# Kernel tuning notes

Hardware: AMD Instinct MI355X
Metric: run time of the kernel (lower is better)

Reference implementation:

```python
import jax, jax.numpy as jnp
import numpy as np

N = 50000      # nodes
E = 800000     # edges (before self-loops)
H = 4          # attention heads
C = 64         # hidden_dim per head
F_IN = 8       # node_features
NEG_SLOPE = 0.2  # PyG GATConv default


def setup_inputs() -> dict:
    key = jax.random.key(0)
    ks = jax.random.split(key, 16)
    def g(k, shape, fan_in):
        return (jax.random.normal(k, shape, jnp.float32) / np.sqrt(fan_in)).astype(jnp.float32)
    x = jax.random.normal(ks[0], (N, F_IN), jnp.float32)
    edge_index = jax.random.randint(ks[1], (2, E), 0, N, dtype=jnp.int32)
    # GATConv params: layer 0 maps F_IN->H*C, layers 1,2 map H*C->H*C
    W0 = g(ks[2], (F_IN, H * C), F_IN)
    Ws = g(ks[3], (2, H * C, H * C), H * C)
    att_src = g(ks[4], (3, H, C), C)
    att_dst = g(ks[5], (3, H, C), C)
    bconv = jnp.zeros((3, H * C), jnp.float32)
    # order / time predictor MLPs: Linear(256,64) -> ReLU -> Linear(64,1)
    ow1 = g(ks[6], (H * C, C), H * C); ob1 = jnp.zeros((C,), jnp.float32)
    ow2 = g(ks[7], (C, 1), C);         ob2 = jnp.zeros((1,), jnp.float32)
    tw1 = g(ks[8], (H * C, C), H * C); tb1 = jnp.zeros((C,), jnp.float32)
    tw2 = g(ks[9], (C, 1), C);         tb2 = jnp.zeros((1,), jnp.float32)
    return {"x": x, "edge_index": edge_index, "W0": W0, "Ws": Ws,
            "att_src": att_src, "att_dst": att_dst, "bconv": bconv,
            "ow1": ow1, "ob1": ob1, "ow2": ow2, "ob2": ob2,
            "tw1": tw1, "tb1": tb1, "tw2": tw2, "tb2": tb2}


def _gat_layer(h_in, src, dst, W, a_src, a_dst, b):
    """PyG-style GATConv (concat heads, eval mode, self-loops already in src/dst)."""
    h = (h_in @ W).reshape(N, H, C)                       # [N,H,C]
    al_s = jnp.einsum('nhc,hc->nh', h, a_src)             # [N,H]
    al_d = jnp.einsum('nhc,hc->nh', h, a_dst)             # [N,H]
    e = jax.nn.leaky_relu(al_s[src] + al_d[dst], NEG_SLOPE)  # [Etot,H]
    m = jax.ops.segment_max(e, dst, num_segments=N)       # segment-softmax over in-edges
    ee = jnp.exp(e - m[dst])
    den = jax.ops.segment_sum(ee, dst, num_segments=N)
    alpha = ee / den[dst]                                 # [Etot,H]
    out = jax.ops.segment_sum(h[src] * alpha[:, :, None], dst, num_segments=N)
    return out.reshape(N, H * C) + b


def reference(x, edge_index, W0, Ws, att_src, att_dst, bconv,
              ow1, ob1, ow2, ob2, tw1, tb1, tw2, tb2):
    loops = jnp.arange(N, dtype=edge_index.dtype)
    src = jnp.concatenate([edge_index[0], loops])
    dst = jnp.concatenate([edge_index[1], loops])
    h = _gat_layer(x, src, dst, W0, att_src[0], att_dst[0], bconv[0])
    h = jax.nn.relu(h)   # dropout is identity in eval
    h = _gat_layer(h, src, dst, Ws[0], att_src[1], att_dst[1], bconv[1])
    h = jax.nn.relu(h)
    h = _gat_layer(h, src, dst, Ws[1], att_src[2], att_dst[2], bconv[2])
    order_scores = jax.nn.relu(h @ ow1 + ob1) @ ow2 + ob2  # [N,1]
    time_scores = jax.nn.relu(h @ tw1 + tb1) @ tw2 + tb2   # [N,1]
    return (order_scores, time_scores)
```

## Files before the change

kernel.cpp:

```cpp
#include <hip/hip_runtime.h>
#include <hip/hip_bf16.h>
#include <hip/hip_fp16.h>

#define NN 50000
#define EE 800000
#define ET 850000
#define HH 4
#define CC 64
#define HC 256

using f16v8 = __attribute__((ext_vector_type(8))) _Float16;
using f32v4 = __attribute__((ext_vector_type(4))) float;

__device__ __forceinline__ int dst_of(const int* ei, int e) {
    return (e < EE) ? ei[EE + e] : (e - EE);
}

__device__ __forceinline__ float4 cvt_h4(uint2 raw) {
    __half2 a = *reinterpret_cast<__half2*>(&raw.x);
    __half2 b = *reinterpret_cast<__half2*>(&raw.y);
    float2 fa = __half22float2(a), fb = __half22float2(b);
    return make_float4(fa.x, fa.y, fb.x, fb.y);
}

__global__ void k_hist(const int* ei, int* cnt) {
    int e = blockIdx.x * blockDim.x + threadIdx.x;
    if (e < ET) atomicAdd(&cnt[dst_of(ei, e)], 1);
}

__global__ void k_scan1(const int* cnt, int* incl, int* bsum) {
    __shared__ int s[256];
    int i = blockIdx.x * 256 + threadIdx.x;
    int v = (i < NN) ? cnt[i] : 0;
    s[threadIdx.x] = v;
    __syncthreads();
    for (int off = 1; off < 256; off <<= 1) {
        int u = (threadIdx.x >= off) ? s[threadIdx.x - off] : 0;
        __syncthreads();
        s[threadIdx.x] += u;
        __syncthreads();
    }
    if (i < NN) incl[i] = s[threadIdx.x];
    if (threadIdx.x == 255) bsum[blockIdx.x] = s[255];
}

__global__ void k_scan2(int* bsum, int nb) {
    __shared__ int s[256];
    int v = (threadIdx.x < nb) ? bsum[threadIdx.x] : 0;
    s[threadIdx.x] = v;
    __syncthreads();
    for (int off = 1; off < 256; off <<= 1) {
        int u = (threadIdx.x >= off) ? s[threadIdx.x - off] : 0;
        __syncthreads();
        s[threadIdx.x] += u;
        __syncthreads();
    }
    if (threadIdx.x < nb) bsum[threadIdx.x] = s[threadIdx.x] - v;
}

__global__ void k_scan3(const int* cnt, const int* incl, const int* bsum,
                        int* row_ptr, int* cur) {
    int i = blockIdx.x * 256 + threadIdx.x;
    if (i < NN) {
        int excl = incl[i] - cnt[i] + bsum[blockIdx.x];
        row_ptr[i] = excl;
        cur[i] = excl;
    }
    if (blockIdx.x == 0 && threadIdx.x == 0) row_ptr[NN] = ET;
}

__global__ void k_scatter(const int* ei, int* cur, int* eidx) {
    int e = blockIdx.x * blockDim.x + threadIdx.x;
    if (e < ET) {
        int d = dst_of(ei, e);
        int pos = atomicAdd(&cur[d], 1);
        eidx[pos] = e;
    }
}

__global__ void k_prep(const float* __restrict__ Ws,
                       const float* __restrict__ ow1, const float* __restrict__ tw1,
                       __half* __restrict__ Wt, __half* __restrict__ Wh) {
    int i = blockIdx.x * 256 + threadIdx.x;
    if (i < 2 * HC * HC) {
        int m = i >> 16;
        int n = (i >> 8) & 255;
        int k = i & 255;
        Wt[i] = __float2half(Ws[m * HC * HC + k * HC + n]);
    }
    int j = i - 2 * HC * HC;
    if (j >= 0 && j < 128 * HC) {
        int c = j >> 8;
        int k = j & 255;
        float v = (c < 64) ? ow1[k * CC + c] : tw1[k * CC + (c - 64)];
        Wh[j] = __float2half(v);
    }
}

#define G0_NODES 16
__global__ __launch_bounds__(256) void k_gemm0(const float* __restrict__ x,
                                               const float* __restrict__ W0,
                                               const float* __restrict__ asrc,
                                               const float* __restrict__ adst,
                                               __half* __restrict__ hg,
                                               float* __restrict__ al_s,
                                               float* __restrict__ al_d) {
    __shared__ float sx[G0_NODES * 8];
    int t = threadIdx.x;
    int n0 = blockIdx.x * G0_NODES;
    float w[8];
#pragma unroll
    for (int k = 0; k < 8; k++) w[k] = W0[k * HC + t];
    float as = asrc[t], ad = adst[t];
    int lane = t & 63, wv = t >> 6;
    if (t < G0_NODES * 8) sx[t] = x[(size_t)n0 * 8 + t];
    __syncthreads();
    for (int ni = 0; ni < G0_NODES; ni++) {
        int n = n0 + ni;
        float acc = 0.f;
#pragma unroll
        for (int k = 0; k < 8; k++) acc += sx[ni * 8 + k] * w[k];
        hg[(size_t)n * HC + t] = __float2half(acc);
        float s = acc * as, d = acc * ad;
        for (int off = 32; off > 0; off >>= 1) {
            s += __shfl_down(s, off, 64);
            d += __shfl_down(d, off, 64);
        }
        if (lane == 0) { al_s[n * HH + wv] = s; al_d[n * HH + wv] = d; }
    }
}

#define GM 128
#define GN 128
#define GK 64
__global__ __launch_bounds__(256) void k_gemmh(const __half* __restrict__ A,
                                               const __half* __restrict__ Bt,
                                               const float* __restrict__ asrc,
                                               const float* __restrict__ adst,
                                               __half* __restrict__ hg,
                                               float* __restrict__ al_s,
                                               float* __restrict__ al_d) {
    __shared__ __half As[GM][GK + 8];
    __shared__ __half Bs[GN][GK + 8];
    int t = threadIdx.x;
    int l = t & 63, wv = t >> 6;
    int wm = wv >> 1, wn = wv & 1;
    int row0 = blockIdx.x * GM;
    int col0 = blockIdx.y * GN;
    f32v4 acc[4][4] = {};
    const __half* Ab = A + (size_t)row0 * HC;
    const __half* Bb = Bt + (size_t)col0 * HC;
    int sr = t >> 3, sc = (t & 7) * 8;
    for (int k0 = 0; k0 < HC; k0 += GK) {
#pragma unroll
        for (int i = 0; i < 4; i++) {
            int rr = sr + i * 32;
            uint4 v = {0u, 0u, 0u, 0u};
            if (row0 + rr < NN) v = *(const uint4*)(Ab + (size_t)rr * HC + k0 + sc);
            *(uint4*)&As[rr][sc] = v;
            *(uint4*)&Bs[rr][sc] = *(const uint4*)(Bb + (size_t)rr * HC + k0 + sc);
        }
        __syncthreads();
#pragma unroll
        for (int kk = 0; kk < GK; kk += 32) {
            f16v8 af[4], bf[4];
#pragma unroll
            for (int i = 0; i < 4; i++)
                af[i] = *(const f16v8*)&As[wm * 64 + i * 16 + (l & 15)][kk + (l >> 4) * 8];
#pragma unroll
            for (int j = 0; j < 4; j++)
                bf[j] = *(const f16v8*)&Bs[wn * 64 + j * 16 + (l & 15)][kk + (l >> 4) * 8];
#pragma unroll
            for (int i = 0; i < 4; i++)
#pragma unroll
                for (int j = 0; j < 4; j++)
                    acc[i][j] = __builtin_amdgcn_mfma_f32_16x16x32_f16(af[i], bf[j], acc[i][j], 0, 0, 0);
        }
        __syncthreads();
    }
    int head = (col0 >> 6) + wn;
    float va[4], vd[4];
#pragma unroll
    for (int j = 0; j < 4; j++) {
        int c = j * 16 + (l & 15);
        va[j] = asrc[head * CC + c];
        vd[j] = adst[head * CC + c];
    }
    int cbase = col0 + wn * 64 + (l & 15);
#pragma unroll
    for (int i = 0; i < 4; i++) {
#pragma unroll
        for (int v = 0; v < 4; v++) {
            int r = row0 + wm * 64 + i * 16 + (l >> 4) * 4 + v;
            bool ok = (r < NN);
            float s = 0.f, d = 0.f;
#pragma unroll
            for (int j = 0; j < 4; j++) {
                float xv = acc[i][j][v];
                s += xv * va[j];
                d += xv * vd[j];
                if (ok) hg[(size_t)r * HC + cbase + j * 16] = __float2half(xv);
            }
            s += __shfl_xor(s, 8, 16); d += __shfl_xor(d, 8, 16);
            s += __shfl_xor(s, 4, 16); d += __shfl_xor(d, 4, 16);
            s += __shfl_xor(s, 2, 16); d += __shfl_xor(d, 2, 16);
            s += __shfl_xor(s, 1, 16); d += __shfl_xor(d, 1, 16);
            if (ok && (l & 15) == 0) {
                al_s[r * HH + head] = s;
                al_d[r * HH + head] = d;
            }
        }
    }
}

__global__ __launch_bounds__(256) void k_fagg(const int* __restrict__ ei,
                                              const int* __restrict__ row_ptr,
                                              const int* __restrict__ eidx,
                                              const float* __restrict__ al_s,
                                              const float* __restrict__ al_d,
                                              const __half* __restrict__ hg,
                                              const float* __restrict__ bias,
                                              __half* __restrict__ out, int do_relu) {
    __shared__ float s_lg[4][HH][72];
    __shared__ int   s_src[4][64];
    int t = threadIdx.x;
    int wv = t >> 6, l = t & 63;
    int n = blockIdx.x * 4 + wv;
    int myh = l >> 4;
    int beg = row_ptr[n], end = row_ptr[n + 1];
    float4 ad = *(const float4*)&al_d[(size_t)n * HH];
    float m = -1e30f, den = 0.f;
    float4 acc = {0.f, 0.f, 0.f, 0.f};
    const __half* hgl = hg + l * 4;

    for (int off = beg; off < end; off += 64) {
        int csize = min(64, end - off);
        float4 lg = {-1e30f, -1e30f, -1e30f, -1e30f};
        int s = 0;
        if (l < csize) {
            int e = eidx[off + l];
            s = (e < EE) ? ei[e] : (e - EE);
            float4 as = *(const float4*)&al_s[(size_t)s * HH];
            float v;
            v = as.x + ad.x; lg.x = (v > 0.f) ? v : 0.2f * v;
            v = as.y + ad.y; lg.y = (v > 0.f) ? v : 0.2f * v;
            v = as.z + ad.z; lg.z = (v > 0.f) ? v : 0.2f * v;
            v = as.w + ad.w; lg.w = (v > 0.f) ? v : 0.2f * v;
        }
        s_src[wv][l] = s;
        s_lg[wv][0][l] = lg.x;
        s_lg[wv][1][l] = lg.y;
        s_lg[wv][2][l] = lg.z;
        s_lg[wv][3][l] = lg.w;
        float4 mx = lg;
#pragma unroll
        for (int dd = 1; dd < 64; dd <<= 1) {
            mx.x = fmaxf(mx.x, __shfl_xor(mx.x, dd, 64));
            mx.y = fmaxf(mx.y, __shfl_xor(mx.y, dd, 64));
            mx.z = fmaxf(mx.z, __shfl_xor(mx.z, dd, 64));
            mx.w = fmaxf(mx.w, __shfl_xor(mx.w, dd, 64));
        }
        float cm = (myh == 0) ? mx.x : (myh == 1) ? mx.y : (myh == 2) ? mx.z : mx.w;
        if (cm > m) {
            float sc = __expf(m - cm);
            acc.x *= sc; acc.y *= sc; acc.z *= sc; acc.w *= sc;
            den *= sc; m = cm;
        }
        const float* lgrow = s_lg[wv][myh];
        const int*   srow  = s_src[wv];
        int k = 0;
        for (; k + 8 <= csize; k += 8) {
            int si[8];
#pragma unroll
            for (int u = 0; u < 8; u++) si[u] = srow[k + u];
            uint2 rw[8];
#pragma unroll
            for (int u = 0; u < 8; u++) rw[u] = *(const uint2*)&hgl[(size_t)si[u] * HC];
            float p[8];
#pragma unroll
            for (int u = 0; u < 8; u++) p[u] = __expf(lgrow[k + u] - m);
#pragma unroll
            for (int u = 0; u < 8; u++) {
                float4 v = cvt_h4(rw[u]);
                den += p[u];
                acc.x += p[u] * v.x;
                acc.y += p[u] * v.y;
                acc.z += p[u] * v.z;
                acc.w += p[u] * v.w;
            }
        }
        for (; k + 4 <= csize; k += 4) {
            int si[4];
#pragma unroll
            for (int u = 0; u < 4; u++) si[u] = srow[k + u];
            uint2 rw[4];
#pragma unroll
            for (int u = 0; u < 4; u++) rw[u] = *(const uint2*)&hgl[(size_t)si[u] * HC];
            float p[4];
#pragma unroll
            for (int u = 0; u < 4; u++) p[u] = __expf(lgrow[k + u] - m);
#pragma unroll
            for (int u = 0; u < 4; u++) {
                float4 v = cvt_h4(rw[u]);
                den += p[u];
                acc.x += p[u] * v.x;
                acc.y += p[u] * v.y;
                acc.z += p[u] * v.z;
                acc.w += p[u] * v.w;
            }
        }
        for (; k < csize; k++) {
            float p = __expf(lgrow[k] - m);
            float4 v = cvt_h4(*(const uint2*)&hgl[(size_t)srow[k] * HC]);
            den += p;
            acc.x += p * v.x; acc.y += p * v.y; acc.z += p * v.z; acc.w += p * v.w;
        }
    }

    float4 b = *(const float4*)&bias[l * 4];
    float inv = 1.f / den;
    float4 o;
    o.x = acc.x * inv + b.x; o.y = acc.y * inv + b.y;
    o.z = acc.z * inv + b.z; o.w = acc.w * inv + b.w;
    if (do_relu) {
        o.x = fmaxf(o.x, 0.f); o.y = fmaxf(o.y, 0.f);
        o.z = fmaxf(o.z, 0.f); o.w = fmaxf(o.w, 0.f);
    }
    union { __half h[4]; uint2 u; } pk;
    pk.h[0] = __float2half(o.x); pk.h[1] = __float2half(o.y);
    pk.h[2] = __float2half(o.z); pk.h[3] = __float2half(o.w);
    *(uint2*)&out[(size_t)n * HC + l * 4] = pk.u;
}

__global__ __launch_bounds__(256) void k_headh(const __half* __restrict__ A,
                                               const __half* __restrict__ Wh,
                                               const float* __restrict__ ob1,
                                               const float* __restrict__ ow2,
                                               const float* __restrict__ ob2,
                                               const float* __restrict__ tb1,
                                               const float* __restrict__ tw2,
                                               const float* __restrict__ tb2,
                                               float* __restrict__ out) {
    __shared__ __half As[GM][GK + 8];
    __shared__ __half Bs[GN][GK + 8];
    int t = threadIdx.x;
    int l = t & 63, wv = t >> 6;
    int wm = wv >> 1, wn = wv & 1;
    int row0 = blockIdx.x * GM;
    f32v4 acc[4][4] = {};
    const __half* Ab = A + (size_t)row0 * HC;
    int sr = t >> 3, sc = (t & 7) * 8;
    for (int k0 = 0; k0 < HC; k0 += GK) {
#pragma unroll
        for (int i = 0; i < 4; i++) {
            int rr = sr + i * 32;
            uint4 v = {0u, 0u, 0u, 0u};
            if (row0 + rr < NN) v = *(const uint4*)(Ab + (size_t)rr * HC + k0 + sc);
            *(uint4*)&As[rr][sc] = v;
            *(uint4*)&Bs[rr][sc] = *(const uint4*)(Wh + (size_t)rr * HC + k0 + sc);
        }
        __syncthreads();
#pragma unroll
        for (int kk = 0; kk < GK; kk += 32) {
            f16v8 af[4], bf[4];
#pragma unroll
            for (int i = 0; i < 4; i++)
                af[i] = *(const f16v8*)&As[wm * 64 + i * 16 + (l & 15)][kk + (l >> 4) * 8];
#pragma unroll
            for (int j = 0; j < 4; j++)
                bf[j] = *(const f16v8*)&Bs[wn * 64 + j * 16 + (l & 15)][kk + (l >> 4) * 8];
#pragma unroll
            for (int i = 0; i < 4; i++)
#pragma unroll
                for (int j = 0; j < 4; j++)
                    acc[i][j] = __builtin_amdgcn_mfma_f32_16x16x32_f16(af[i], bf[j], acc[i][j], 0, 0, 0);
        }
        __syncthreads();
    }
    float b1[4], w2[4];
#pragma unroll
    for (int j = 0; j < 4; j++) {
        int c = j * 16 + (l & 15);
        b1[j] = wn ? tb1[c] : ob1[c];
        w2[j] = wn ? tw2[c] : ow2[c];
    }
    float b2 = wn ? tb2[0] : ob2[0];
#pragma unroll
    for (int i = 0; i < 4; i++) {
#pragma unroll
        for (int v = 0; v < 4; v++) {
            int r = row0 + wm * 64 + i * 16 + (l >> 4) * 4 + v;
            float s = 0.f;
#pragma unroll
            for (int j = 0; j < 4; j++)
                s += fmaxf(acc[i][j][v] + b1[j], 0.f) * w2[j];
            s += __shfl_xor(s, 8, 16);
            s += __shfl_xor(s, 4, 16);
            s += __shfl_xor(s, 2, 16);
            s += __shfl_xor(s, 1, 16);
            if ((l & 15) == 0 && r < NN)
                out[(size_t)(wn ? NN : 0) + r] = s + b2;
        }
    }
}

extern "C" void kernel_launch(void* const* d_in, const int* in_sizes, int n_in,
                              void* d_out, int out_size, void* d_ws, size_t ws_size,
                              hipStream_t stream) {
    const float* x      = (const float*)d_in[0];
    const int*   ei     = (const int*)d_in[1];
    const float* W0     = (const float*)d_in[2];
    const float* Ws     = (const float*)d_in[3];
    const float* attsrc = (const float*)d_in[4];
    const float* attdst = (const float*)d_in[5];
    const float* bconv  = (const float*)d_in[6];
    const float* ow1 = (const float*)d_in[7];
    const float* ob1 = (const float*)d_in[8];
    const float* ow2 = (const float*)d_in[9];
    const float* ob2 = (const float*)d_in[10];
    const float* tw1 = (const float*)d_in[11];
    const float* tb1 = (const float*)d_in[12];
    const float* tw2 = (const float*)d_in[13];
    const float* tb2 = (const float*)d_in[14];
    float* outp = (float*)d_out;

    char* ws = (char*)d_ws;
    size_t off = 0;
    auto alloc = [&](size_t bytes) -> void* {
        void* p = ws + off;
        off += (bytes + 255) & ~(size_t)255;
        return p;
    };
    __half*   hA      = (__half*)alloc(sizeof(__half) * NN * HC);
    __half*   hB16    = (__half*)alloc(sizeof(__half) * NN * HC);
    float*    al_s    = (float*)alloc(sizeof(float) * NN * HH);
    float*    al_d    = (float*)alloc(sizeof(float) * NN * HH);
    int*      cnt     = (int*)alloc(sizeof(int) * NN);
    int*      incl    = (int*)alloc(sizeof(int) * NN);
    int*      bsum    = (int*)alloc(sizeof(int) * 256);
    int*      row_ptr = (int*)alloc(sizeof(int) * (NN + 1));
    int*      cur     = (int*)alloc(sizeof(int) * NN);
    int*      eidx    = (int*)alloc(sizeof(int) * ET);
    __half*   Wt      = (__half*)alloc(sizeof(__half) * 2 * HC * HC);
    __half*   Wh      = (__half*)alloc(sizeof(__half) * 128 * HC);
    (void)ws_size; (void)in_sizes; (void)n_in; (void)out_size;

    hipMemsetAsync(cnt, 0, sizeof(int) * NN, stream);
    int nbScan = (NN + 255) / 256;
    k_hist<<<(ET + 255) / 256, 256, 0, stream>>>(ei, cnt);
    k_scan1<<<nbScan, 256, 0, stream>>>(cnt, incl, bsum);
    k_scan2<<<1, 256, 0, stream>>>(bsum, nbScan);
    k_scan3<<<nbScan, 256, 0, stream>>>(cnt, incl, bsum, row_ptr, cur);
    k_scatter<<<(ET + 255) / 256, 256, 0, stream>>>(ei, cur, eidx);
    k_prep<<<(2 * HC * HC + 128 * HC + 255) / 256, 256, 0, stream>>>(Ws, ow1, tw1, Wt, Wh);

    for (int l = 0; l < 3; l++) {
        if (l == 0) {
            k_gemm0<<<NN / G0_NODES, 256, 0, stream>>>(x, W0, attsrc, attdst,
                                                       hA, al_s, al_d);
        } else {
            dim3 grid((NN + GM - 1) / GM, 2);
            k_gemmh<<<grid, 256, 0, stream>>>(hB16, Wt + (size_t)(l - 1) * HC * HC,
                                              attsrc + l * HC, attdst + l * HC,
                                              hA, al_s, al_d);
        }
        k_fagg<<<NN / 4, 256, 0, stream>>>(ei, row_ptr, eidx, al_s, al_d, hA,
                                           bconv + l * HC, hB16, (l < 2) ? 1 : 0);
    }

    k_headh<<<(NN + GM - 1) / GM, 256, 0, stream>>>(hB16, Wh, ob1, ow2, ob2,
                                                    tb1, tw2, tb2, outp);
}
```

Measured before the change: 433.8 us.

## Split wave into half-waves with 16-byte gathers and prefetched edge pipeline

The attention aggregation kernel now splits each wave into two 32-lane halves. Each half handles alternating edges and each lane gathers 8 fp16 features with a single 16-byte load instead of 4 features with an 8-byte load. A rolling four-deep register prefetch loads the next neighbor rows while the current ones are accumulated, and the two halves are combined with a cross-half shuffle before the output is written. The aim is fewer, wider memory transactions and more gather latency hidden per wave. The cost is higher register pressure, an extra reduction step, and half the lanes sitting idle during the store.

```diff
diff --git a/kernel.cpp b/kernel.cpp
--- a/kernel.cpp
+++ b/kernel.cpp
@@ -225,13 +225,15 @@
     __shared__ int   s_src[4][64];
     int t = threadIdx.x;
     int wv = t >> 6, l = t & 63;
+    int half = l >> 5;
+    int lc = l & 31;
+    int myh = lc >> 3;
     int n = blockIdx.x * 4 + wv;
-    int myh = l >> 4;
     int beg = row_ptr[n], end = row_ptr[n + 1];
     float4 ad = *(const float4*)&al_d[(size_t)n * HH];
     float m = -1e30f, den = 0.f;
-    float4 acc = {0.f, 0.f, 0.f, 0.f};
-    const __half* hgl = hg + l * 4;
+    float acc[8] = {0.f, 0.f, 0.f, 0.f, 0.f, 0.f, 0.f, 0.f};
+    const __half* hgl = hg + lc * 8;
 
     for (int off = beg; off < end; off += 64) {
         int csize = min(64, end - off);
@@ -263,73 +265,77 @@
         float cm = (myh == 0) ? mx.x : (myh == 1) ? mx.y : (myh == 2) ? mx.z : mx.w;
         if (cm > m) {
             float sc = __expf(m - cm);
-            acc.x *= sc; acc.y *= sc; acc.z *= sc; acc.w *= sc;
+#pragma unroll
+            for (int u = 0; u < 8; u++) acc[u] *= sc;
             den *= sc; m = cm;
         }
         const float* lgrow = s_lg[wv][myh];
         const int*   srow  = s_src[wv];
-        int k = 0;
-        for (; k + 8 <= csize; k += 8) {
-            int si[8];
-#pragma unroll
-            for (int u = 0; u < 8; u++) si[u] = srow[k + u];
-            uint2 rw[8];
-#pragma unroll
-            for (int u = 0; u < 8; u++) rw[u] = *(const uint2*)&hgl[(size_t)si[u] * HC];
-            float p[8];
-#pragma unroll
-            for (int u = 0; u < 8; u++) p[u] = __expf(lgrow[k + u] - m);
-#pragma unroll
-            for (int u = 0; u < 8; u++) {
-                float4 v = cvt_h4(rw[u]);
-                den += p[u];
-                acc.x += p[u] * v.x;
-                acc.y += p[u] * v.y;
-                acc.z += p[u] * v.z;
-                acc.w += p[u] * v.w;
+        int npairs = (csize + 1) >> 1;
+        int pmain = npairs & ~3;
+        uint4 rw[4];
+        float lgv[4];
+        if (pmain) {
+#pragma unroll
+            for (int u = 0; u < 4; u++) {
+                int e = 2 * u + half;
+                rw[u] = *(const uint4*)&hgl[(size_t)srow[e] * HC];
+                lgv[u] = lgrow[e];
             }
-        }
-        for (; k + 4 <= csize; k += 4) {
-            int si[4];
-#pragma unroll
-            for (int u = 0; u < 4; u++) si[u] = srow[k + u];
-            uint2 rw[4];
-#pragma unroll
-            for (int u = 0; u < 4; u++) rw[u] = *(const uint2*)&hgl[(size_t)si[u] * HC];
-            float p[4];
-#pragma unroll
-            for (int u = 0; u < 4; u++) p[u] = __expf(lgrow[k + u] - m);
-#pragma unroll
-            for (int u = 0; u < 4; u++) {
-                float4 v = cvt_h4(rw[u]);
-                den += p[u];
-                acc.x += p[u] * v.x;
-                acc.y += p[u] * v.y;
-                acc.z += p[u] * v.z;
-                acc.w += p[u] * v.w;
+            for (int p0 = 0; p0 < pmain; p0 += 4) {
+#pragma unroll
+                for (int u = 0; u < 4; u++) {
+                    float pv = __expf(lgv[u] - m);
+                    float4 va = cvt_h4(make_uint2(rw[u].x, rw[u].y));
+                    float4 vb = cvt_h4(make_uint2(rw[u].z, rw[u].w));
+                    int pn = p0 + 4 + u;
+                    if (pn < pmain) {
+                        int e = 2 * pn + half;
+                        rw[u] = *(const uint4*)&hgl[(size_t)srow[e] * HC];
+                        lgv[u] = lgrow[e];
+                    }
+                    den += pv;
+                    acc[0] += pv * va.x; acc[1] += pv * va.y;
+                    acc[2] += pv * va.z; acc[3] += pv * va.w;
+                    acc[4] += pv * vb.x; acc[5] += pv * vb.y;
+                    acc[6] += pv * vb.z; acc[7] += pv * vb.w;
+                }
             }
         }
-        for (; k < csize; k++) {
-            float p = __expf(lgrow[k] - m);
-            float4 v = cvt_h4(*(const uint2*)&hgl[(size_t)srow[k] * HC]);
-            den += p;
-            acc.x += p * v.x; acc.y += p * v.y; acc.z += p * v.z; acc.w += p * v.w;
-        }
-    }
-
-    float4 b = *(const float4*)&bias[l * 4];
-    float inv = 1.f / den;
-    float4 o;
-    o.x = acc.x * inv + b.x; o.y = acc.y * inv + b.y;
-    o.z = acc.z * inv + b.z; o.w = acc.w * inv + b.w;
-    if (do_relu) {
-        o.x = fmaxf(o.x, 0.f); o.y = fmaxf(o.y, 0.f);
-        o.z = fmaxf(o.z, 0.f); o.w = fmaxf(o.w, 0.f);
-    }
-    union { __half h[4]; uint2 u; } pk;
-    pk.h[0] = __float2half(o.x); pk.h[1] = __float2half(o.y);
-    pk.h[2] = __float2half(o.z); pk.h[3] = __float2half(o.w);
-    *(uint2*)&out[(size_t)n * HC + l * 4] = pk.u;
+        for (int p = pmain; p < npairs; p++) {
+            int e = 2 * p + half;
+            float pv = __expf(lgrow[e] - m);
+            uint4 r = *(const uint4*)&hgl[(size_t)srow[e] * HC];
+            float4 va = cvt_h4(make_uint2(r.x, r.y));
+            float4 vb = cvt_h4(make_uint2(r.z, r.w));
+            den += pv;
+            acc[0] += pv * va.x; acc[1] += pv * va.y;
+            acc[2] += pv * va.z; acc[3] += pv * va.w;
+            acc[4] += pv * vb.x; acc[5] += pv * vb.y;
+            acc[6] += pv * vb.z; acc[7] += pv * vb.w;
+        }
+    }
+
+    den += __shfl_xor(den, 32, 64);
+#pragma unroll
+    for (int u = 0; u < 8; u++) acc[u] += __shfl_xor(acc[u], 32, 64);
+    if (l < 32) {
+        float4 b0 = *(const float4*)&bias[lc * 8];
+        float4 b1 = *(const float4*)&bias[lc * 8 + 4];
+        float inv = 1.f / den;
+        float o[8];
+        o[0] = acc[0] * inv + b0.x; o[1] = acc[1] * inv + b0.y;
+        o[2] = acc[2] * inv + b0.z; o[3] = acc[3] * inv + b0.w;
+        o[4] = acc[4] * inv + b1.x; o[5] = acc[5] * inv + b1.y;
+        o[6] = acc[6] * inv + b1.z; o[7] = acc[7] * inv + b1.w;
+        union { __half h[8]; uint4 u4; } pk;
+#pragma unroll
+        for (int u = 0; u < 8; u++) {
+            float ov = do_relu ? fmaxf(o[u], 0.f) : o[u];
+            pk.h[u] = __float2half(ov);
+        }
+        *(uint4*)&out[(size_t)n * HC + lc * 8] = pk.u4;
+    }
 }
 
 __global__ __launch_bounds__(256) void k_headh(const __half* __restrict__ A,
```

Result: slower. 455.6 us (+5.0%).
